# Kernel optimization log

Hardware: AMD Instinct MI355X
Metric: run time of the kernel (lower is better)

The kernel has to match this reference:

```python
import jax, jax.numpy as jnp
import numpy as np

B, T, C = 4, 2048, 1024
L = 256
H = 16
HS = C // H  # 64

def setup_inputs() -> dict:
    key = jax.random.key(0)
    ks = jax.random.split(key, 6)
    s = 0.02
    return {
        "x": jax.random.normal(ks[0], (B, T, C), dtype=jnp.float32),
        "Wq": jax.random.normal(ks[1], (C, C), dtype=jnp.float32) * s,
        "W_kv_down": jax.random.normal(ks[2], (C, L), dtype=jnp.float32) * s,
        "W_k_up": jax.random.normal(ks[3], (L, C), dtype=jnp.float32) * s,
        "W_v_up": jax.random.normal(ks[4], (L, C), dtype=jnp.float32) * s,
        "W_out": jax.random.normal(ks[5], (C, C), dtype=jnp.float32) * s,
    }

def reference(x, Wq, W_kv_down, W_k_up, W_v_up, W_out):
    # x: [B,T,C]
    q = (x @ Wq).reshape(B, T, H, HS).transpose(0, 2, 1, 3)        # [B,H,T,HS]
    latent_kv = x @ W_kv_down                                       # [B,T,L]
    k = (latent_kv @ W_k_up).reshape(B, T, H, HS).transpose(0, 2, 1, 3)
    v = (latent_kv @ W_v_up).reshape(B, T, H, HS).transpose(0, 2, 1, 3)
    att = jnp.einsum('bhtd,bhsd->bhts', q, k) / jnp.sqrt(jnp.float32(HS))
    causal = jnp.tril(jnp.ones((T, T), dtype=bool))
    att = jnp.where(causal[None, None], att, jnp.float32(-jnp.inf))
    att = jax.nn.softmax(att, axis=-1)
    y = jnp.einsum('bhts,bhsd->bhtd', att, v)                       # [B,H,T,HS]
    y = y.transpose(0, 2, 1, 3).reshape(B, T, C)
    return y @ W_out
```

## Files before the change

kernel.cpp:

```cpp
#include <hip/hip_runtime.h>
#include <cstddef>
#include <cstdint>

#define BB 4
#define TT 2048
#define CC 1024
#define LL 256
#define HH 16
#define DD 64
#define QLD (CC + LL)

typedef __attribute__((ext_vector_type(8))) short s16x8;
typedef __attribute__((ext_vector_type(4))) float f32x4;

static __device__ inline unsigned short f2bf(float f) {
    union { float f; unsigned u; } v; v.f = f;
    unsigned r = v.u + 0x7fffu + ((v.u >> 16) & 1u);
    return (unsigned short)(r >> 16);
}

static __device__ inline float fast_exp2(float x) {
#if __has_builtin(__builtin_amdgcn_exp2f)
    return __builtin_amdgcn_exp2f(x);
#else
    return exp2f(x);
#endif
}

static __device__ inline unsigned pack_bf16_trunc(float lo, float hi) {
    union { float f; unsigned u; } a, b;
    a.f = lo; b.f = hi;
    return __builtin_amdgcn_perm(b.u, a.u, 0x07060302u);
}

#define GLDS16(g, l)                                             \
    __builtin_amdgcn_global_load_lds(                            \
        (__attribute__((address_space(1))) void*)(g),            \
        (__attribute__((address_space(3))) void*)(l), 16, 0, 0)

extern "C" __global__ __launch_bounds__(256)
void fused_cvt(const float* __restrict__ x, unsigned short* __restrict__ xb,
               const float* __restrict__ Wq, const float* __restrict__ Wkv,
               const float* __restrict__ Wk, const float* __restrict__ Wv,
               const float* __restrict__ Wo,
               unsigned short* __restrict__ W1t, unsigned short* __restrict__ W2t,
               unsigned short* __restrict__ Wot, float qscale) {
    __shared__ unsigned short Ts[64][72];
    const int t = threadIdx.x;
    int blk = blockIdx.x;
    if (blk < 8192) {
        const int i = blk * 256 + t;
        const float4 v = ((const float4*)x)[i];
        ushort4 o;
        o.x = f2bf(v.x); o.y = f2bf(v.y); o.z = f2bf(v.z); o.w = f2bf(v.w);
        ((ushort4*)xb)[i] = o;
        return;
    }
    blk -= 8192;
    const float* W; unsigned short* Wt; int K, N; float scale; int tile;
    if (blk < 256)      { W = Wq;  Wt = W1t;                      K = CC; N = CC; scale = qscale; tile = blk; }
    else if (blk < 320) { W = Wkv; Wt = W1t + (size_t)CC * CC;    K = CC; N = LL; scale = 1.f;    tile = blk - 256; }
    else if (blk < 384) { W = Wk;  Wt = W2t;                      K = LL; N = CC; scale = 1.f;    tile = blk - 320; }
    else if (blk < 448) { W = Wv;  Wt = W2t + (size_t)CC * LL;    K = LL; N = CC; scale = 1.f;    tile = blk - 384; }
    else                { W = Wo;  Wt = Wot;                      K = CC; N = CC; scale = 1.f;    tile = blk - 448; }
    const int ktiles = K >> 6;
    const int k0 = (tile % ktiles) * 64, n0 = (tile / ktiles) * 64;
#pragma unroll
    for (int l = 0; l < 4; ++l) {
        const int idx = t + l * 256;
        const int r = idx >> 4, c4 = (idx & 15) * 4;
        const float4 v = *(const float4*)(W + (size_t)(k0 + r) * N + n0 + c4);
        Ts[c4 + 0][r] = f2bf(v.x * scale); Ts[c4 + 1][r] = f2bf(v.y * scale);
        Ts[c4 + 2][r] = f2bf(v.z * scale); Ts[c4 + 3][r] = f2bf(v.w * scale);
    }
    __syncthreads();
#pragma unroll
    for (int l = 0; l < 2; ++l) {
        const int idx = t + l * 256;
        const int n = idx >> 3, seg = idx & 7;
        *(s16x8*)(Wt + (size_t)(n0 + n) * K + k0 + seg * 8) = *(const s16x8*)&Ts[n][seg * 8];
    }
}

template <int MODE>
__global__ __launch_bounds__(256)
void bgemm(const unsigned short* __restrict__ A, const unsigned short* __restrict__ Bt,
           void* __restrict__ Cv, void* __restrict__ Cv2,
           int M, int N, int K, int lda, int ldc) {
    __shared__ unsigned short As[128][64];
    __shared__ unsigned short Bs[128][64];
    const int t = threadIdx.x;
    const int w = t >> 6, lane = t & 63, quad = lane >> 4, l16 = lane & 15;
    const int wm = w & 1, wn = w >> 1;
    const int row0 = blockIdx.y * 128, col0 = blockIdx.x * 128;
    const int sr = lane >> 3;
    const int sc = ((lane & 7) ^ sr) * 8;

    f32x4 acc[4][4];
#pragma unroll
    for (int i = 0; i < 4; ++i)
#pragma unroll
        for (int j = 0; j < 4; ++j) acc[i][j] = (f32x4){0.f, 0.f, 0.f, 0.f};

    const unsigned short* Ab = A + (size_t)(row0 + w * 32 + sr) * lda + sc;
    const unsigned short* Bb = Bt + (size_t)(col0 + w * 32 + sr) * K + sc;

    for (int k0 = 0; k0 < K; k0 += 64) {
#pragma unroll
        for (int c = 0; c < 4; ++c) {
            GLDS16(Ab + (size_t)(c * 8) * lda + k0, &As[w * 32 + c * 8][0]);
            GLDS16(Bb + (size_t)(c * 8) * K + k0, &Bs[w * 32 + c * 8][0]);
        }
        __syncthreads();
#pragma unroll
        for (int kk = 0; kk < 2; ++kk) {
            s16x8 af[4], bfr[4];
#pragma unroll
            for (int mt = 0; mt < 4; ++mt)
                af[mt] = *(const s16x8*)
                    &As[wm * 64 + mt * 16 + l16][((kk * 4 + quad) ^ (l16 & 7)) * 8];
#pragma unroll
            for (int nt = 0; nt < 4; ++nt)
                bfr[nt] = *(const s16x8*)
                    &Bs[wn * 64 + nt * 16 + l16][((kk * 4 + quad) ^ (l16 & 7)) * 8];
#pragma unroll
            for (int mt = 0; mt < 4; ++mt)
#pragma unroll
                for (int nt = 0; nt < 4; ++nt)
                    acc[mt][nt] = __builtin_amdgcn_mfma_f32_16x16x32_bf16(
                        af[mt], bfr[nt], acc[mt][nt], 0, 0, 0);
        }
        __syncthreads();
    }

    if constexpr (MODE == 0) {
        float* C = (float*)Cv;
#pragma unroll
        for (int mt = 0; mt < 4; ++mt)
#pragma unroll
            for (int nt = 0; nt < 4; ++nt)
#pragma unroll
                for (int r = 0; r < 4; ++r)
                    C[(size_t)(row0 + wm * 64 + mt * 16 + quad * 4 + r) * ldc +
                      col0 + wn * 64 + nt * 16 + l16] = acc[mt][nt][r];
    } else if constexpr (MODE == 1) {
        unsigned short* C = (unsigned short*)Cv;
#pragma unroll
        for (int mt = 0; mt < 4; ++mt)
#pragma unroll
            for (int nt = 0; nt < 4; ++nt)
#pragma unroll
                for (int r = 0; r < 4; ++r)
                    C[(size_t)(row0 + wm * 64 + mt * 16 + quad * 4 + r) * ldc +
                      col0 + wn * 64 + nt * 16 + l16] = f2bf(acc[mt][nt][r]);
    } else {
        if (col0 < CC) {
            unsigned short* C = (unsigned short*)Cv;
#pragma unroll
            for (int mt = 0; mt < 4; ++mt)
#pragma unroll
                for (int nt = 0; nt < 4; ++nt)
#pragma unroll
                    for (int r = 0; r < 4; ++r)
                        C[(size_t)(row0 + wm * 64 + mt * 16 + quad * 4 + r) * ldc +
                          col0 + wn * 64 + nt * 16 + l16] = f2bf(acc[mt][nt][r]);
        } else {
            __shared__ unsigned short Tb[64][136];
            unsigned short* vt = (unsigned short*)Cv2;
            const int b   = row0 >> 11;
            const int tl0 = row0 & 2047;
#pragma unroll
            for (int h = 0; h < 2; ++h) {
                if (wn == h) {
#pragma unroll
                    for (int mt = 0; mt < 4; ++mt)
#pragma unroll
                        for (int nt = 0; nt < 4; ++nt)
#pragma unroll
                            for (int r = 0; r < 4; ++r)
                                Tb[nt * 16 + l16][wm * 64 + mt * 16 + quad * 4 + r] =
                                    f2bf(acc[mt][nt][r]);
                }
                __syncthreads();
                const int head = ((col0 - CC) >> 6) + h;
#pragma unroll
                for (int l = 0; l < 4; ++l) {
                    const int idx = t + l * 256;
                    const int dv = idx >> 4, seg = idx & 15;
                    *(s16x8*)(vt + (((size_t)b * HH + head) * DD + dv) * TT + tl0 + seg * 8) =
                        *(const s16x8*)&Tb[dv][seg * 8];
                }
                __syncthreads();
            }
        }
    }
}

extern "C" __global__ __launch_bounds__(256)
void mla_attn2(const unsigned short* __restrict__ q,
               const unsigned short* __restrict__ k,
               const unsigned short* __restrict__ vt,
               unsigned short* __restrict__ y) {
    __shared__ unsigned short Ks[64][64];
    __shared__ unsigned short Vs[64][64];
    __shared__ unsigned short Ps[4][32][72];

    const int bh = blockIdx.x;
    const int qt2 = (gridDim.y - 1) - blockIdx.y;
    const int b = bh >> 4, h = bh & 15;
    const int t0 = qt2 * 128;
    const int t = threadIdx.x;
    const int w = t >> 6, lane = t & 63, quad = lane >> 4, l16 = lane & 15;
    const int qw0 = t0 + w * 32;
    const int swz = ((lane & 7) ^ ((lane >> 3) & 7)) * 8;
    const int lrow = lane >> 3;

    const unsigned short* kb0 = k + ((size_t)b * TT) * CC + h * DD;
    const unsigned short* vb0 = vt + ((size_t)(b * HH + h)) * DD * TT;

    s16x8 qf[2][2];
#pragma unroll
    for (int qs = 0; qs < 2; ++qs)
#pragma unroll
        for (int kh = 0; kh < 2; ++kh)
            qf[qs][kh] = *(const s16x8*)(q + ((size_t)b * TT + qw0 + qs * 16 + l16) * QLD +
                                         h * DD + kh * 32 + quad * 8);

    f32x4 o[2][4];
    float lsum[2] = {0.f, 0.f};
#pragma unroll
    for (int qs = 0; qs < 2; ++qs)
#pragma unroll
        for (int nt = 0; nt < 4; ++nt) o[qs][nt] = (f32x4){0.f, 0.f, 0.f, 0.f};

    const int nkt = 2 * qt2 + 2;
    for (int kt = 0; kt < nkt; ++kt) {
        const int s0 = kt * 64;
#pragma unroll
        for (int c = 0; c < 2; ++c) {
            const int g = w * 2 + c;
            const int row = g * 8 + lrow;
            GLDS16(kb0 + (size_t)(s0 + row) * CC + swz, &Ks[g * 8][0]);
            GLDS16(vb0 + (size_t)row * TT + s0 + swz, &Vs[g * 8][0]);
        }
        __syncthreads();

        if (s0 <= qw0 + 31) {
            f32x4 st[2][4];
#pragma unroll
            for (int nt = 0; nt < 4; ++nt) {
                const int key = nt * 16 + l16;
                const s16x8 kf0 = *(const s16x8*)&Ks[key][((0 + quad) ^ (l16 & 7)) * 8];
                const s16x8 kf1 = *(const s16x8*)&Ks[key][((4 + quad) ^ (l16 & 7)) * 8];
#pragma unroll
                for (int qs = 0; qs < 2; ++qs) {
                    f32x4 acc = (f32x4){0.f, 0.f, 0.f, 0.f};
                    acc = __builtin_amdgcn_mfma_f32_16x16x32_bf16(kf0, qf[qs][0], acc, 0, 0, 0);
                    acc = __builtin_amdgcn_mfma_f32_16x16x32_bf16(kf1, qf[qs][1], acc, 0, 0, 0);
                    st[qs][nt] = acc;
                }
            }

            const bool maskedTile = (s0 + 63 > qw0);
#pragma unroll
            for (int qs = 0; qs < 2; ++qs) {
                const int qidx = qw0 + qs * 16 + l16;
#pragma unroll
                for (int nt = 0; nt < 4; ++nt) {
                    const int key0 = s0 + nt * 16 + quad * 4;
                    float p[4];
#pragma unroll
                    for (int r = 0; r < 4; ++r) {
                        float sv = st[qs][nt][r];
                        if (maskedTile && (key0 + r > qidx)) sv = -1e30f;
                        const float e = fast_exp2(sv);
                        p[r] = e;
                        lsum[qs] += e;
                    }
                    const unsigned lo = pack_bf16_trunc(p[0], p[1]);
                    const unsigned hi = pack_bf16_trunc(p[2], p[3]);
                    uint2 pk; pk.x = lo; pk.y = hi;
                    *(uint2*)&Ps[w][qs * 16 + l16][nt * 16 + quad * 4] = pk;
                }
            }

            s16x8 pf[2][2];
#pragma unroll
            for (int qs = 0; qs < 2; ++qs)
#pragma unroll
                for (int kh = 0; kh < 2; ++kh)
                    pf[qs][kh] = *(const s16x8*)&Ps[w][qs * 16 + l16][kh * 32 + quad * 8];
#pragma unroll
            for (int nt = 0; nt < 4; ++nt) {
                const int dv = nt * 16 + l16;
                const s16x8 vf0 = *(const s16x8*)&Vs[dv][((0 + quad) ^ (l16 & 7)) * 8];
                const s16x8 vf1 = *(const s16x8*)&Vs[dv][((4 + quad) ^ (l16 & 7)) * 8];
#pragma unroll
                for (int qs = 0; qs < 2; ++qs) {
                    o[qs][nt] = __builtin_amdgcn_mfma_f32_16x16x32_bf16(pf[qs][0], vf0,
                                                                        o[qs][nt], 0, 0, 0);
                    o[qs][nt] = __builtin_amdgcn_mfma_f32_16x16x32_bf16(pf[qs][1], vf1,
                                                                        o[qs][nt], 0, 0, 0);
                }
            }
        }
        __syncthreads();
    }

    float lfull[2];
#pragma unroll
    for (int qs = 0; qs < 2; ++qs) {
        float s = lsum[qs];
        s += __shfl_xor(s, 16);
        s += __shfl_xor(s, 32);
        lfull[qs] = s;
    }

#pragma unroll
    for (int qs = 0; qs < 2; ++qs) {
#pragma unroll
        for (int r = 0; r < 4; ++r) {
            const float inv = 1.f / __shfl(lfull[qs], quad * 4 + r);
            unsigned short* yb = y + ((size_t)b * TT + qw0 + qs * 16 + quad * 4 + r) * CC +
                                 h * DD + l16;
#pragma unroll
            for (int nt = 0; nt < 4; ++nt)
                yb[nt * 16] = f2bf(o[qs][nt][r] * inv);
        }
    }
}

extern "C" void kernel_launch(void* const* d_in, const int* in_sizes, int n_in,
                              void* d_out, int out_size, void* d_ws, size_t ws_size,
                              hipStream_t stream) {
    const float* x   = (const float*)d_in[0];
    const float* Wq  = (const float*)d_in[1];
    const float* Wkv = (const float*)d_in[2];
    const float* Wk  = (const float*)d_in[3];
    const float* Wv  = (const float*)d_in[4];
    const float* Wo  = (const float*)d_in[5];
    float* out = (float*)d_out;

    const int M = BB * TT;
    unsigned short* p = (unsigned short*)d_ws;
    unsigned short* xb    = p; p += (size_t)M * CC;
    unsigned short* qlatb = p; p += (size_t)M * QLD;
    unsigned short* kb    = p; p += (size_t)M * CC;
    unsigned short* vtb   = p; p += (size_t)M * CC;
    unsigned short* yb    = p; p += (size_t)M * CC;
    unsigned short* W1t   = p; p += (size_t)QLD * CC;
    unsigned short* W2t   = p; p += (size_t)(2 * CC) * LL;
    unsigned short* Wot   = p; p += (size_t)CC * CC;

    const float qscale = 0.125f * 1.44269504f;

    fused_cvt<<<8896, 256, 0, stream>>>(x, xb, Wq, Wkv, Wk, Wv, Wo,
                                        W1t, W2t, Wot, qscale);
    bgemm<1><<<dim3(QLD / 128, M / 128), 256, 0, stream>>>(
        xb, W1t, qlatb, nullptr, M, QLD, CC, CC, QLD);
    bgemm<3><<<dim3(2 * CC / 128, M / 128), 256, 0, stream>>>(
        qlatb + CC, W2t, kb, vtb, M, 2 * CC, LL, QLD, CC);
    mla_attn2<<<dim3(BB * HH, TT / 128), 256, 0, stream>>>(qlatb, kb, vtb, yb);
    bgemm<0><<<dim3(CC / 128, M / 128), 256, 0, stream>>>(
        yb, Wot, out, nullptr, M, CC, CC, CC, CC);
}
```

Baseline: 236.9 us.

## Rewrite attention to register-direct K/V loads with pairwise causal balancing, swizzle GEMM blocks

```diff
diff --git a/kernel.cpp b/kernel.cpp
--- a/kernel.cpp
+++ b/kernel.cpp
@@ -92,7 +92,13 @@
     const int t = threadIdx.x;
     const int w = t >> 6, lane = t & 63, quad = lane >> 4, l16 = lane & 15;
     const int wm = w & 1, wn = w >> 1;
-    const int row0 = blockIdx.y * 128, col0 = blockIdx.x * 128;
+
+    int wg = blockIdx.y * gridDim.x + blockIdx.x;
+    const int nwg = gridDim.x * gridDim.y;
+    if ((nwg & 7) == 0) wg = (wg & 7) * (nwg >> 3) + (wg >> 3);
+    const int bx = wg % gridDim.x, by = wg / gridDim.x;
+    const int row0 = by * 128, col0 = bx * 128;
+
     const int sr = lane >> 3;
     const int sc = ((lane & 7) ^ sr) * 8;
 
@@ -196,138 +202,156 @@
     }
 }
 
-extern "C" __global__ __launch_bounds__(256)
-void mla_attn2(const unsigned short* __restrict__ q,
+extern "C" __global__ __launch_bounds__(256, 2)
+void mla_attn5(const unsigned short* __restrict__ q,
                const unsigned short* __restrict__ k,
                const unsigned short* __restrict__ vt,
                unsigned short* __restrict__ y) {
-    __shared__ unsigned short Ks[64][64];
-    __shared__ unsigned short Vs[64][64];
-    __shared__ unsigned short Ps[4][32][72];
-
     const int bh = blockIdx.x;
-    const int qt2 = (gridDim.y - 1) - blockIdx.y;
     const int b = bh >> 4, h = bh & 15;
-    const int t0 = qt2 * 128;
-    const int t = threadIdx.x;
-    const int w = t >> 6, lane = t & 63, quad = lane >> 4, l16 = lane & 15;
-    const int qw0 = t0 + w * 32;
-    const int swz = ((lane & 7) ^ ((lane >> 3) & 7)) * 8;
-    const int lrow = lane >> 3;
-
-    const unsigned short* kb0 = k + ((size_t)b * TT) * CC + h * DD;
-    const unsigned short* vb0 = vt + ((size_t)(b * HH + h)) * DD * TT;
-
-    s16x8 qf[2][2];
-#pragma unroll
-    for (int qs = 0; qs < 2; ++qs)
-#pragma unroll
-        for (int kh = 0; kh < 2; ++kh)
-            qf[qs][kh] = *(const s16x8*)(q + ((size_t)b * TT + qw0 + qs * 16 + l16) * QLD +
-                                         h * DD + kh * 32 + quad * 8);
-
-    f32x4 o[2][4];
-    float lsum[2] = {0.f, 0.f};
-#pragma unroll
-    for (int qs = 0; qs < 2; ++qs)
-#pragma unroll
-        for (int nt = 0; nt < 4; ++nt) o[qs][nt] = (f32x4){0.f, 0.f, 0.f, 0.f};
-
-    const int nkt = 2 * qt2 + 2;
-    for (int kt = 0; kt < nkt; ++kt) {
-        const int s0 = kt * 64;
-#pragma unroll
-        for (int c = 0; c < 2; ++c) {
-            const int g = w * 2 + c;
-            const int row = g * 8 + lrow;
-            GLDS16(kb0 + (size_t)(s0 + row) * CC + swz, &Ks[g * 8][0]);
-            GLDS16(vb0 + (size_t)row * TT + s0 + swz, &Vs[g * 8][0]);
-        }
-        __syncthreads();
-
-        if (s0 <= qw0 + 31) {
-            f32x4 st[2][4];
-#pragma unroll
-            for (int nt = 0; nt < 4; ++nt) {
-                const int key = nt * 16 + l16;
-                const s16x8 kf0 = *(const s16x8*)&Ks[key][((0 + quad) ^ (l16 & 7)) * 8];
-                const s16x8 kf1 = *(const s16x8*)&Ks[key][((4 + quad) ^ (l16 & 7)) * 8];
-#pragma unroll
-                for (int qs = 0; qs < 2; ++qs) {
-                    f32x4 acc = (f32x4){0.f, 0.f, 0.f, 0.f};
-                    acc = __builtin_amdgcn_mfma_f32_16x16x32_bf16(kf0, qf[qs][0], acc, 0, 0, 0);
-                    acc = __builtin_amdgcn_mfma_f32_16x16x32_bf16(kf1, qf[qs][1], acc, 0, 0, 0);
-                    st[qs][nt] = acc;
-                }
+    const int w = threadIdx.x >> 6;
+    const int pidx = blockIdx.y * 4 + w;
+    const int lane = threadIdx.x & 63, quad = lane >> 4, l16 = lane & 15;
+
+    const unsigned short* kbl = k + ((size_t)b * TT) * CC + h * DD + quad * 8 +
+                                (size_t)l16 * CC;
+    const unsigned short* vbl = vt + ((size_t)(b * HH + h)) * DD * TT + quad * 8 +
+                                (size_t)l16 * TT;
+
+#define LOAD_FRAGS(KF, VF, s0_)                                                \
+    do {                                                                       \
+        _Pragma("unroll")                                                      \
+        for (int nt_ = 0; nt_ < 4; ++nt_) {                                    \
+            const unsigned short* kr_ = kbl + (size_t)((s0_) + nt_ * 16) * CC; \
+            KF[nt_][0] = *(const s16x8*)(kr_);                                 \
+            KF[nt_][1] = *(const s16x8*)(kr_ + 32);                            \
+            const unsigned short* vr_ = vbl + (size_t)(nt_ * 16) * TT + (s0_); \
+            VF[nt_][0] = *(const s16x8*)(vr_);                                 \
+            VF[nt_][1] = *(const s16x8*)(vr_ + 32);                            \
+        }                                                                      \
+    } while (0)
+
+#define COMPUTE_TILE(KF, VF, s0_)                                              \
+    do {                                                                       \
+        const bool masked_ = ((s0_) + 63 > qw0);             \
+        _Pragma("unroll")                                                      \
+        for (int qs_ = 0; qs_ < 2; ++qs_) {                                    \
+            f32x4 st_[4];                                                      \
+            _Pragma("unroll")                                                  \
+            for (int nt_ = 0; nt_ < 4; ++nt_) {                                \
+                f32x4 a_ = (f32x4){0.f, 0.f, 0.f, 0.f};                        \
+                a_ = __builtin_amdgcn_mfma_f32_16x16x32_bf16(                  \
+                    KF[nt_][0], qf[qs_][0], a_, 0, 0, 0);                      \
+                a_ = __builtin_amdgcn_mfma_f32_16x16x32_bf16(                  \
+                    KF[nt_][1], qf[qs_][1], a_, 0, 0, 0);                      \
+                st_[nt_] = a_;                                                 \
+            }                                                                  \
+            const int qidx_ = qw0 + qs_ * 16 + l16;                            \
+            unsigned pc_[4][2];                                                \
+            float ts_ = 0.f;                                                   \
+            _Pragma("unroll")                                                  \
+            for (int nt_ = 0; nt_ < 4; ++nt_) {                                \
+                const int key0_ = (s0_) + nt_ * 16 + quad * 4;                 \
+                float pv_[4];                                                  \
+                _Pragma("unroll")                                              \
+                for (int r_ = 0; r_ < 4; ++r_) {                               \
+                    float sv_ = st_[nt_][r_];                                  \
+                    if (masked_ && (key0_ + r_ > qidx_)) sv_ = -1e30f;         \
+                    pv_[r_] = fast_exp2(sv_);                                  \
+                }                                                              \
+                ts_ += (pv_[0] + pv_[1]) + (pv_[2] + pv_[3]);                  \
+                pc_[nt_][0] = pack_bf16_trunc(pv_[0], pv_[1]);                 \
+                pc_[nt_][1] = pack_bf16_trunc(pv_[2], pv_[3]);                 \
+            }                                                                  \
+            lsum[qs_] += ts_;                                                  \
+            s16x8 pf_[2];                                                      \
+            _Pragma("unroll")                                                  \
+            for (int kh_ = 0; kh_ < 2; ++kh_) {                                \
+                auto sa_ = __builtin_amdgcn_permlane32_swap(                   \
+                    (int)pc_[2 * kh_ + 0][0], (int)pc_[2 * kh_ + 1][0],        \
+                    false, false);                                             \
+                auto w02_ = __builtin_amdgcn_permlane16_swap(                  \
+                    sa_[0], sa_[1], false, false);                             \
+                auto sb_ = __builtin_amdgcn_permlane32_swap(                   \
+                    (int)pc_[2 * kh_ + 0][1], (int)pc_[2 * kh_ + 1][1],        \
+                    false, false);                                             \
+                auto w13_ = __builtin_amdgcn_permlane16_swap(                  \
+                    sb_[0], sb_[1], false, false);                             \
+                union { unsigned u[4]; s16x8 v; } fu_;                         \
+                fu_.u[0] = (unsigned)w02_[0];                  \
+                fu_.u[1] = (unsigned)w13_[0];                  \
+                fu_.u[2] = (unsigned)w02_[1];                  \
+                fu_.u[3] = (unsigned)w13_[1];                  \
+                pf_[kh_] = fu_.v;                                              \
+            }                                                                  \
+            _Pragma("unroll")                                                  \
+            for (int nt_ = 0; nt_ < 4; ++nt_) {                                \
+                o[qs_][nt_] = __builtin_amdgcn_mfma_f32_16x16x32_bf16(         \
+                    pf_[0], VF[nt_][0], o[qs_][nt_], 0, 0, 0);                 \
+                o[qs_][nt_] = __builtin_amdgcn_mfma_f32_16x16x32_bf16(         \
+                    pf_[1], VF[nt_][1], o[qs_][nt_], 0, 0, 0);                 \
+            }                                                                  \
+        }                                                                      \
+    } while (0)
+
+#pragma unroll 1
+    for (int item = 0; item < 2; ++item) {
+        const int qt = (item == 0) ? (63 - pidx) : pidx;
+        const int qw0 = qt * 32;
+        const int nkt = (qt >> 1) + 1;
+
+        s16x8 qf[2][2];
+#pragma unroll
+        for (int qs = 0; qs < 2; ++qs)
+#pragma unroll
+            for (int kh = 0; kh < 2; ++kh)
+                qf[qs][kh] = *(const s16x8*)(q + ((size_t)b * TT + qw0 + qs * 16 + l16) * QLD +
+                                             h * DD + kh * 32 + quad * 8);
+
+        f32x4 o[2][4];
+        float lsum[2] = {0.f, 0.f};
+#pragma unroll
+        for (int qs = 0; qs < 2; ++qs)
+#pragma unroll
+            for (int nt = 0; nt < 4; ++nt) o[qs][nt] = (f32x4){0.f, 0.f, 0.f, 0.f};
+
+        s16x8 kfA[4][2], vfA[4][2], kfB[4][2], vfB[4][2];
+        LOAD_FRAGS(kfA, vfA, 0);
+        int kt = 0;
+#pragma unroll 1
+        for (;;) {
+            if (kt + 1 < nkt) LOAD_FRAGS(kfB, vfB, (kt + 1) * 64);
+            COMPUTE_TILE(kfA, vfA, kt * 64);
+            if (++kt >= nkt) break;
+            if (kt + 1 < nkt) LOAD_FRAGS(kfA, vfA, (kt + 1) * 64);
+            COMPUTE_TILE(kfB, vfB, kt * 64);
+            if (++kt >= nkt) break;
+        }
+
+        float lfull[2];
+#pragma unroll
+        for (int qs = 0; qs < 2; ++qs) {
+            float s = lsum[qs];
+            s += __shfl_xor(s, 16);
+            s += __shfl_xor(s, 32);
+            lfull[qs] = s;
+        }
+
+#pragma unroll
+        for (int qs = 0; qs < 2; ++qs) {
+#pragma unroll
+            for (int r = 0; r < 4; ++r) {
+                const float inv = 1.f / __shfl(lfull[qs], quad * 4 + r);
+                unsigned short* yb = y + ((size_t)b * TT + qw0 + qs * 16 + quad * 4 + r) * CC +
+                                     h * DD + l16;
+#pragma unroll
+                for (int nt = 0; nt < 4; ++nt)
+                    yb[nt * 16] = f2bf(o[qs][nt][r] * inv);
             }
-
-            const bool maskedTile = (s0 + 63 > qw0);
-#pragma unroll
-            for (int qs = 0; qs < 2; ++qs) {
-                const int qidx = qw0 + qs * 16 + l16;
-#pragma unroll
-                for (int nt = 0; nt < 4; ++nt) {
-                    const int key0 = s0 + nt * 16 + quad * 4;
-                    float p[4];
-#pragma unroll
-                    for (int r = 0; r < 4; ++r) {
-                        float sv = st[qs][nt][r];
-                        if (maskedTile && (key0 + r > qidx)) sv = -1e30f;
-                        const float e = fast_exp2(sv);
-                        p[r] = e;
-                        lsum[qs] += e;
-                    }
-                    const unsigned lo = pack_bf16_trunc(p[0], p[1]);
-                    const unsigned hi = pack_bf16_trunc(p[2], p[3]);
-                    uint2 pk; pk.x = lo; pk.y = hi;
-                    *(uint2*)&Ps[w][qs * 16 + l16][nt * 16 + quad * 4] = pk;
-                }
-            }
-
-            s16x8 pf[2][2];
-#pragma unroll
-            for (int qs = 0; qs < 2; ++qs)
-#pragma unroll
-                for (int kh = 0; kh < 2; ++kh)
-                    pf[qs][kh] = *(const s16x8*)&Ps[w][qs * 16 + l16][kh * 32 + quad * 8];
-#pragma unroll
-            for (int nt = 0; nt < 4; ++nt) {
-                const int dv = nt * 16 + l16;
-                const s16x8 vf0 = *(const s16x8*)&Vs[dv][((0 + quad) ^ (l16 & 7)) * 8];
-                const s16x8 vf1 = *(const s16x8*)&Vs[dv][((4 + quad) ^ (l16 & 7)) * 8];
-#pragma unroll
-                for (int qs = 0; qs < 2; ++qs) {
-                    o[qs][nt] = __builtin_amdgcn_mfma_f32_16x16x32_bf16(pf[qs][0], vf0,
-                                                                        o[qs][nt], 0, 0, 0);
-                    o[qs][nt] = __builtin_amdgcn_mfma_f32_16x16x32_bf16(pf[qs][1], vf1,
-                                                                        o[qs][nt], 0, 0, 0);
-                }
-            }
-        }
-        __syncthreads();
-    }
-
-    float lfull[2];
-#pragma unroll
-    for (int qs = 0; qs < 2; ++qs) {
-        float s = lsum[qs];
-        s += __shfl_xor(s, 16);
-        s += __shfl_xor(s, 32);
-        lfull[qs] = s;
-    }
-
-#pragma unroll
-    for (int qs = 0; qs < 2; ++qs) {
-#pragma unroll
-        for (int r = 0; r < 4; ++r) {
-            const float inv = 1.f / __shfl(lfull[qs], quad * 4 + r);
-            unsigned short* yb = y + ((size_t)b * TT + qw0 + qs * 16 + quad * 4 + r) * CC +
-                                 h * DD + l16;
-#pragma unroll
-            for (int nt = 0; nt < 4; ++nt)
-                yb[nt * 16] = f2bf(o[qs][nt][r] * inv);
-        }
-    }
+        }
+    }
+#undef LOAD_FRAGS
+#undef COMPUTE_TILE
 }
 
 extern "C" void kernel_launch(void* const* d_in, const int* in_sizes, int n_in,
@@ -360,7 +384,7 @@
         xb, W1t, qlatb, nullptr, M, QLD, CC, CC, QLD);
     bgemm<3><<<dim3(2 * CC / 128, M / 128), 256, 0, stream>>>(
         qlatb + CC, W2t, kb, vtb, M, 2 * CC, LL, QLD, CC);
-    mla_attn2<<<dim3(BB * HH, TT / 128), 256, 0, stream>>>(qlatb, kb, vtb, yb);
+    mla_attn5<<<dim3(BB * HH, 8), 256, 0, stream>>>(qlatb, kb, vtb, yb);
     bgemm<0><<<dim3(CC / 128, M / 128), 256, 0, stream>>>(
         yb, Wot, out, nullptr, M, CC, CC, CC, CC);
 }
```

New measurement: 307.7 us. 1.3x slower.
